# Kernel optimization log

Hardware: AMD Instinct MI355X
Metric: run time of the kernel (lower is better)

The kernel has to match this reference:

```python
import jax, jax.numpy as jnp
import numpy as np

K_HOPS = 3  # spektral TAGConv default
BN_EPS = 1e-3  # keras BatchNormalization default epsilon


def _propagate(x, edge_src, edge_dst, edge_weight, n_nodes):
    # y[dst] += w * x[src]  (sparse adjacency @ x)
    msg = x[edge_src] * edge_weight[:, None]
    return jax.ops.segment_sum(msg, edge_dst, num_segments=n_nodes)


def _tag_conv(x, edge_src, edge_dst, edge_weight, W, b):
    n = x.shape[0]
    hops = [x]
    h = x
    for _ in range(K_HOPS):
        h = _propagate(h, edge_src, edge_dst, edge_weight, n)
        hops.append(h)
    # concat hops along features then dense combine: [N, F*(K+1)] @ [F*(K+1), C]
    return jnp.concatenate(hops, axis=-1) @ W + b


def setup_inputs() -> dict:
    key = jax.random.key(0)
    ks = jax.random.split(key, 6)
    N, F, E, H, L = 20000, 2000, 640000, 128, 15
    x = jax.random.normal(ks[0], (N, F), dtype=jnp.float32)
    edge_src = jax.random.randint(ks[1], (E,), 0, N, dtype=jnp.int32)
    edge_dst = jax.random.randint(ks[2], (E,), 0, N, dtype=jnp.int32)
    # normalized adjacency weights, roughly 1/avg_degree scale
    edge_weight = jax.random.uniform(ks[3], (E,), dtype=jnp.float32) / 32.0
    W1 = jax.random.normal(ks[4], (F * (K_HOPS + 1), H), dtype=jnp.float32) * (1.0 / np.sqrt(F * (K_HOPS + 1)))
    b1 = jnp.zeros((H,), dtype=jnp.float32)
    gamma = jnp.ones((H,), dtype=jnp.float32)
    beta = jnp.zeros((H,), dtype=jnp.float32)
    moving_mean = jnp.zeros((H,), dtype=jnp.float32)
    moving_var = jnp.ones((H,), dtype=jnp.float32)
    W2 = jax.random.normal(ks[5], (H * (K_HOPS + 1), L), dtype=jnp.float32) * (1.0 / np.sqrt(H * (K_HOPS + 1)))
    b2 = jnp.zeros((L,), dtype=jnp.float32)
    return {"x": x, "edge_src": edge_src, "edge_dst": edge_dst, "edge_weight": edge_weight,
            "W1": W1, "b1": b1, "gamma": gamma, "beta": beta,
            "moving_mean": moving_mean, "moving_var": moving_var, "W2": W2, "b2": b2}


def reference(x, edge_src, edge_dst, edge_weight, W1, b1, gamma, beta,
              moving_mean, moving_var, W2, b2):
    # training=False: Dropout is identity, BN uses moving statistics
    h = _tag_conv(x, edge_src, edge_dst, edge_weight, W1, b1)
    h = (h - moving_mean) * jax.lax.rsqrt(moving_var + BN_EPS) * gamma + beta
    h = jax.nn.relu(h)
    z = _tag_conv(h, edge_src, edge_dst, edge_weight, W2, b2)
    return z
```

## Files before the change

kernel.cpp:

```cpp
#include <hip/hip_runtime.h>
#include <hip/hip_bf16.h>
#include <cstdint>
#include <cstddef>

#define N_NODES 20000
#define F_IN    2000
#define H_DIM   128
#define L_DIM   15
#define K_PAD   2048
#define YS      384
#define BM      128
#define BN      64
#define BK      32
#define I_TILES 157

typedef __attribute__((ext_vector_type(4))) float f32x4;
typedef __attribute__((ext_vector_type(8))) short s16x8;
typedef __attribute__((ext_vector_type(8))) unsigned short u16x8;

__device__ __forceinline__ unsigned short f2bf(float f) {
  unsigned int u = __float_as_uint(f);
  u += 0x7fff + ((u >> 16) & 1);
  return (unsigned short)(u >> 16);
}

__device__ __forceinline__ unsigned int pkbf(float a, float b) {
  union { __hip_bfloat162 h; unsigned int u; } cv;
  cv.h = __float22bfloat162_rn(make_float2(a, b));
  return cv.u;
}

__device__ __forceinline__ float2 bf2f(unsigned int u) {
  float2 r;
  r.x = __uint_as_float(u << 16);
  r.y = __uint_as_float(u & 0xffff0000u);
  return r;
}

__global__ __launch_bounds__(256) void k_cvt_x(const float* __restrict__ x,
                                               unsigned short* __restrict__ xb) {
  unsigned int t = blockIdx.x * 256u + threadIdx.x;
  unsigned int row = t >> 8;
  unsigned int colB = (t & 255u) * 8u;
  u16x8 o = {0, 0, 0, 0, 0, 0, 0, 0};
  if (colB < F_IN) {
    const float4 a = *(const float4*)(x + (size_t)row * F_IN + colB);
    const float4 b = *(const float4*)(x + (size_t)row * F_IN + colB + 4);
    o[0] = f2bf(a.x); o[1] = f2bf(a.y); o[2] = f2bf(a.z); o[3] = f2bf(a.w);
    o[4] = f2bf(b.x); o[5] = f2bf(b.y); o[6] = f2bf(b.z); o[7] = f2bf(b.w);
  }
  *(u16x8*)(xb + (size_t)t * 8) = o;
}

__global__ __launch_bounds__(256) void k_cvt_w1(const float* __restrict__ W1,
                                                unsigned short* __restrict__ bt) {
  __shared__ unsigned short tile[128 * 67];
  const int hop = blockIdx.x >> 5;
  const int k0  = (blockIdx.x & 31) * 64;
  const int t = threadIdx.x;
#pragma unroll
  for (int it = 0; it < 8; ++it) {
    int f4 = it * 256 + t;
    int r  = f4 >> 5;
    int c4 = f4 & 31;
    int k = k0 + r;
    float4 v = make_float4(0.f, 0.f, 0.f, 0.f);
    if (k < F_IN) v = *(const float4*)(W1 + (size_t)(hop * F_IN + k) * H_DIM + c4 * 4);
    tile[(c4 * 4 + 0) * 67 + r] = f2bf(v.x);
    tile[(c4 * 4 + 1) * 67 + r] = f2bf(v.y);
    tile[(c4 * 4 + 2) * 67 + r] = f2bf(v.z);
    tile[(c4 * 4 + 3) * 67 + r] = f2bf(v.w);
  }
  __syncthreads();
  const int c = t >> 1, kh = (t & 1) * 32;
  unsigned short* dst = bt + (size_t)(hop * 128 + c) * K_PAD + k0 + kh;
  const unsigned short* srcp = tile + c * 67 + kh;
#pragma unroll
  for (int q = 0; q < 4; ++q) {
    u16x8 o;
#pragma unroll
    for (int e = 0; e < 8; ++e) o[e] = srcp[q * 8 + e];
    *(u16x8*)(dst + q * 8) = o;
  }
}

__global__ __launch_bounds__(256) void k_gemm1(const unsigned short* __restrict__ A,
                                               const unsigned short* __restrict__ B,
                                               float* __restrict__ Y,
                                               unsigned short* __restrict__ Yb3) {
  __shared__ unsigned short As[BM * BK];
  __shared__ unsigned short Bs[BN * BK];
  const int b = blockIdx.x;
  const int i_tile = (b & 7) + 8 * (b >> 6);
  const int j_tile = (b >> 3) & 7;
  if (i_tile >= I_TILES) return;
  const int rowA0 = i_tile * BM;
  const int colB0 = j_tile * BN;
  const int tid  = threadIdx.x;
  const int lane = tid & 63;
  const int wave = tid >> 6;
  const int wm = (wave >> 1) * 64;
  const int wn = (wave & 1) * 32;
  const int quad = lane >> 4;
  const int l15  = lane & 15;
  f32x4 acc[4][2] = {};

  for (int kt = 0; kt < K_PAD; kt += BK) {
#pragma unroll
    for (int r = 0; r < 2; ++r) {
      int c = r * 256 + tid;
      int row = c >> 2;
      int kc = (c & 3) * 8;
      const unsigned short* ga = A + (size_t)(rowA0 + row) * K_PAD + kt + kc;
      __builtin_amdgcn_global_load_lds((const __attribute__((address_space(1))) void*)ga,
                                       (__attribute__((address_space(3))) void*)(As + c * 8),
                                       16, 0, 0);
    }
    {
      int c = tid;
      int row = c >> 2;
      int kc = (c & 3) * 8;
      const unsigned short* gb = B + (size_t)(colB0 + row) * K_PAD + kt + kc;
      __builtin_amdgcn_global_load_lds((const __attribute__((address_space(1))) void*)gb,
                                       (__attribute__((address_space(3))) void*)(Bs + c * 8),
                                       16, 0, 0);
    }
    __syncthreads();
    s16x8 af[4], bfr[2];
#pragma unroll
    for (int i = 0; i < 4; ++i)
      af[i] = *(const s16x8*)(As + (wm + i * 16 + l15) * BK + quad * 8);
#pragma unroll
    for (int j = 0; j < 2; ++j)
      bfr[j] = *(const s16x8*)(Bs + (wn + j * 16 + l15) * BK + quad * 8);
#pragma unroll
    for (int i = 0; i < 4; ++i)
#pragma unroll
      for (int j = 0; j < 2; ++j)
        acc[i][j] = __builtin_amdgcn_mfma_f32_16x16x32_bf16(af[i], bfr[j], acc[i][j], 0, 0, 0);
    __syncthreads();
  }

#pragma unroll
  for (int i = 0; i < 4; ++i) {
    int row0 = rowA0 + wm + i * 16 + quad * 4;
#pragma unroll
    for (int j = 0; j < 2; ++j) {
      int gcol = colB0 + wn + j * 16 + l15;
#pragma unroll
      for (int r = 0; r < 4; ++r) {
        int row = row0 + r;
        if (row < N_NODES) {
          if (j_tile < 6)
            Y[(size_t)row * YS + gcol] = acc[i][j][r];
          else
            Yb3[(size_t)row * H_DIM + (gcol - 384)] = f2bf(acc[i][j][r]);
        }
      }
    }
  }
}

__global__ __launch_bounds__(256) void k_hist(const int* __restrict__ dst,
                                              int* __restrict__ deg, int E) {
  int i = blockIdx.x * 256 + threadIdx.x;
  int e = i * 4;
  if (e + 4 <= E) {
    int4 d4 = *(const int4*)(dst + e);
    atomicAdd(&deg[d4.x], 1); atomicAdd(&deg[d4.y], 1);
    atomicAdd(&deg[d4.z], 1); atomicAdd(&deg[d4.w], 1);
  } else {
    for (; e < E; ++e) atomicAdd(&deg[dst[e]], 1);
  }
}

__global__ __launch_bounds__(1024) void k_scan(const int* __restrict__ deg,
                                               int* __restrict__ rowStart,
                                               int* __restrict__ cursor) {
  __shared__ int sums[1024];
  const int t = threadIdx.x;
  const int chunk = (N_NODES + 1023) / 1024;
  int lo = t * chunk;
  int hi = lo + chunk; if (hi > N_NODES) hi = N_NODES;
  int s = 0;
  for (int i = lo; i < hi; ++i) s += deg[i];
  sums[t] = s;
  __syncthreads();
  for (int off = 1; off < 1024; off <<= 1) {
    int v = sums[t];
    int u = (t >= off) ? sums[t - off] : 0;
    __syncthreads();
    sums[t] = v + u;
    __syncthreads();
  }
  int run = sums[t] - s;
  for (int i = lo; i < hi; ++i) {
    rowStart[i] = run; cursor[i] = run; run += deg[i];
  }
  if (t == 1023) rowStart[N_NODES] = run;
}

__global__ __launch_bounds__(256) void k_scatter(const int* __restrict__ src,
                                                 const int* __restrict__ dst,
                                                 const float* __restrict__ w,
                                                 int* cursor,
                                                 int2* __restrict__ eSW, int E) {
  int e = blockIdx.x * 256 + threadIdx.x;
  if (e >= E) return;
  int p = atomicAdd(&cursor[dst[e]], 1);
  eSW[p] = make_int2(src[e], __float_as_int(w[e]));
}

__global__ __launch_bounds__(256) void k_prop128e(const int* __restrict__ rowStart,
    const int2* __restrict__ eSW,
    const unsigned short* __restrict__ gsrc,
    const float* __restrict__ addv, int addStride, int addOff,
    unsigned short* __restrict__ outb, float* __restrict__ outf,
    const float* __restrict__ b1, const float* __restrict__ gamma,
    const float* __restrict__ beta, const float* __restrict__ mean,
    const float* __restrict__ var, int doBN) {
  const int lane = threadIdx.x & 63;
  const int wave = threadIdx.x >> 6;
  const int h   = lane >> 5;
  const int sub = lane & 31;
  const int d = blockIdx.x * 4 + wave;
  const int s0 = rowStart[d], s1 = rowStart[d + 1];
  f32x4 acc = {0.f, 0.f, 0.f, 0.f};

  const int nc = (s1 - s0) >> 4;
  int j = s0;
  int2 ed[8];
  if (nc > 0) {
#pragma unroll
    for (int i = 0; i < 8; ++i) ed[i] = eSW[j + 2 * i + h];
  }
  for (int c = 0; c < nc; ++c) {
    uint2 g[8];
#pragma unroll
    for (int i = 0; i < 8; ++i)
      g[i] = *(const uint2*)(gsrc + (size_t)ed[i].x * H_DIM + sub * 4);
    int2 edn[8];
    if (c + 1 < nc) {
#pragma unroll
      for (int i = 0; i < 8; ++i) edn[i] = eSW[j + 16 + 2 * i + h];
    }
#pragma unroll
    for (int i = 0; i < 8; ++i) {
      float w = __int_as_float(ed[i].y);
      float2 lo = bf2f(g[i].x), hi = bf2f(g[i].y);
      acc.x = fmaf(w, lo.x, acc.x); acc.y = fmaf(w, lo.y, acc.y);
      acc.z = fmaf(w, hi.x, acc.z); acc.w = fmaf(w, hi.y, acc.w);
    }
    if (c + 1 < nc) {
#pragma unroll
      for (int i = 0; i < 8; ++i) ed[i] = edn[i];
    }
    j += 16;
  }
  for (int t = s0 + nc * 16 + h; t < s1; t += 2) {
    int2 e = eSW[t];
    uint2 g = *(const uint2*)(gsrc + (size_t)e.x * H_DIM + sub * 4);
    float w = __int_as_float(e.y);
    float2 lo = bf2f(g.x), hi = bf2f(g.y);
    acc.x = fmaf(w, lo.x, acc.x); acc.y = fmaf(w, lo.y, acc.y);
    acc.z = fmaf(w, hi.x, acc.z); acc.w = fmaf(w, hi.y, acc.w);
  }
  acc.x += __shfl_xor(acc.x, 32);
  acc.y += __shfl_xor(acc.y, 32);
  acc.z += __shfl_xor(acc.z, 32);
  acc.w += __shfl_xor(acc.w, 32);
  if (h) return;
  const int c4 = sub * 4;
  float4 av = *(const float4*)(addv + (size_t)d * addStride + addOff + c4);
  float r0 = av.x + acc.x, r1 = av.y + acc.y;
  float r2 = av.z + acc.z, r3 = av.w + acc.w;
  if (doBN) {
    float4 bb = *(const float4*)(b1 + c4);
    float4 gg = *(const float4*)(gamma + c4);
    float4 be = *(const float4*)(beta + c4);
    float4 mm = *(const float4*)(mean + c4);
    float4 vv = *(const float4*)(var + c4);
    r0 = (r0 + bb.x - mm.x) * rsqrtf(vv.x + 1e-3f) * gg.x + be.x;
    r1 = (r1 + bb.y - mm.y) * rsqrtf(vv.y + 1e-3f) * gg.y + be.y;
    r2 = (r2 + bb.z - mm.z) * rsqrtf(vv.z + 1e-3f) * gg.z + be.z;
    r3 = (r3 + bb.w - mm.w) * rsqrtf(vv.w + 1e-3f) * gg.w + be.w;
    r0 = r0 > 0.f ? r0 : 0.f; r1 = r1 > 0.f ? r1 : 0.f;
    r2 = r2 > 0.f ? r2 : 0.f; r3 = r3 > 0.f ? r3 : 0.f;
    *(float4*)(outf + (size_t)d * H_DIM + c4) = make_float4(r0, r1, r2, r3);
  } else {
    *(uint2*)(outb + (size_t)d * H_DIM + c4) = make_uint2(pkbf(r0, r1), pkbf(r2, r3));
  }
}

__global__ __launch_bounds__(256) void k_gemm2(const float* __restrict__ Hh,
                                               const float* __restrict__ W2,
                                               float* __restrict__ Y2) {
  __shared__ float w2s[512 * 15];
  for (int i = threadIdx.x; i < 512 * 15; i += 256) w2s[i] = W2[i];
  __syncthreads();
  const int c = threadIdx.x & 63;
  const int d = blockIdx.x * 4 + (threadIdx.x >> 6);
  if (c >= 60 || d >= N_NODES) return;
  const int hop = c / 15, j = c % 15;
  const float4* hr4 = (const float4*)(Hh + (size_t)d * H_DIM);
  float acc = 0.f;
#pragma unroll 8
  for (int k4 = 0; k4 < 32; ++k4) {
    float4 h = hr4[k4];
    const float* wp = w2s + ((hop << 7) + k4 * 4) * 15 + j;
    acc = fmaf(h.x, wp[0],  acc);
    acc = fmaf(h.y, wp[15], acc);
    acc = fmaf(h.z, wp[30], acc);
    acc = fmaf(h.w, wp[45], acc);
  }
  Y2[(size_t)d * 60 + c] = acc;
}

__global__ __launch_bounds__(256) void k_prop15(const int* __restrict__ rowStart,
    const int2* __restrict__ eSW,
    const float* __restrict__ in, int inStride, int inOff,
    const float* __restrict__ addv, int addStride, int addOff,
    const float* __restrict__ bias, float* __restrict__ out) {
  const int f = threadIdx.x & 15;
  const int d = blockIdx.x * 16 + (threadIdx.x >> 4);
  if (f >= 15) return;
  const int s0 = rowStart[d], s1 = rowStart[d + 1];
  float acc = 0.f;
  int j = s0;
  for (; j + 4 <= s1; j += 4) {
    int2 e0 = eSW[j], e1 = eSW[j + 1], e2 = eSW[j + 2], e3 = eSW[j + 3];
    float v0 = in[(size_t)e0.x * inStride + inOff + f];
    float v1 = in[(size_t)e1.x * inStride + inOff + f];
    float v2 = in[(size_t)e2.x * inStride + inOff + f];
    float v3 = in[(size_t)e3.x * inStride + inOff + f];
    acc = fmaf(__int_as_float(e0.y), v0, acc);
    acc = fmaf(__int_as_float(e1.y), v1, acc);
    acc = fmaf(__int_as_float(e2.y), v2, acc);
    acc = fmaf(__int_as_float(e3.y), v3, acc);
  }
  for (; j < s1; ++j) {
    int2 e = eSW[j];
    acc = fmaf(__int_as_float(e.y), in[(size_t)e.x * inStride + inOff + f], acc);
  }
  float b = bias ? bias[f] : 0.f;
  out[(size_t)d * 15 + f] = addv[(size_t)d * addStride + addOff + f] + acc + b;
}

extern "C" void kernel_launch(void* const* d_in, const int* in_sizes, int n_in,
                              void* d_out, int out_size, void* d_ws, size_t ws_size,
                              hipStream_t stream) {
  const float* x     = (const float*)d_in[0];
  const int*   esrc  = (const int*)d_in[1];
  const int*   edst  = (const int*)d_in[2];
  const float* ew    = (const float*)d_in[3];
  const float* W1    = (const float*)d_in[4];
  const float* b1    = (const float*)d_in[5];
  const float* gamma = (const float*)d_in[6];
  const float* beta  = (const float*)d_in[7];
  const float* mmean = (const float*)d_in[8];
  const float* mvar  = (const float*)d_in[9];
  const float* W2    = (const float*)d_in[10];
  const float* b2    = (const float*)d_in[11];
  const int E = in_sizes[1];
  char* ws = (char*)d_ws;

  unsigned short* xb  = (unsigned short*)(ws);
  float*          Y   = (float*)(ws + 81920000);
  unsigned short* Yb3 = (unsigned short*)(ws + 112640000);
  unsigned short* w1r = (unsigned short*)(ws + 117760000);
  int2*           eSW = (int2*)(ws + 119857152);
  int*       deg      = (int*)(ws + 124977152);
  int*       rowStart = (int*)(ws + 125057280);
  int*       cursor   = (int*)(ws + 125137408);
  unsigned short* P   = (unsigned short*)(ws);
  unsigned short* Q   = (unsigned short*)(ws + 5120000);
  float*          Hb  = (float*)(ws + 10240000);
  float*          Y2  = (float*)(ws + 20480000);
  float*          zP  = (float*)(ws + 25280000);
  float*          zQ  = (float*)(ws + 26480000);
  float*          zout = (float*)d_out;

  hipMemsetAsync(deg, 0, N_NODES * sizeof(int), stream);

  k_hist<<<(E / 4 + 255) / 256 + 1, 256, 0, stream>>>(edst, deg, E);
  k_scan<<<1, 1024, 0, stream>>>(deg, rowStart, cursor);
  k_scatter<<<(E + 255) / 256, 256, 0, stream>>>(esrc, edst, ew, cursor, eSW, E);

  k_cvt_x<<<(N_NODES * K_PAD / 8) / 256, 256, 0, stream>>>(x, xb);
  k_cvt_w1<<<128, 256, 0, stream>>>(W1, w1r);
  k_gemm1<<<1280, 256, 0, stream>>>(xb, w1r, Y, Yb3);

  k_prop128e<<<N_NODES / 4, 256, 0, stream>>>(rowStart, eSW, Yb3, Y, YS, 256,
                                              P, nullptr, b1, gamma, beta, mmean, mvar, 0);
  k_prop128e<<<N_NODES / 4, 256, 0, stream>>>(rowStart, eSW, P, Y, YS, 128,
                                              Q, nullptr, b1, gamma, beta, mmean, mvar, 0);
  k_prop128e<<<N_NODES / 4, 256, 0, stream>>>(rowStart, eSW, Q, Y, YS, 0,
                                              nullptr, Hb, b1, gamma, beta, mmean, mvar, 1);

  k_gemm2<<<N_NODES / 4, 256, 0, stream>>>(Hb, W2, Y2);
  k_prop15<<<N_NODES / 16, 256, 0, stream>>>(rowStart, eSW, Y2, 60, 45, Y2, 60, 30, nullptr, zP);
  k_prop15<<<N_NODES / 16, 256, 0, stream>>>(rowStart, eSW, zP, 15, 0, Y2, 60, 15, nullptr, zQ);
  k_prop15<<<N_NODES / 16, 256, 0, stream>>>(rowStart, eSW, zQ, 15, 0, Y2, 60, 0, b2, zout);
}
```

Baseline: 604.6 us.

## Pad CSR rows to multiples of 16 and widen per-lane gathers to 16 bytes

The CSR build now rounds each node's edge segment up to a multiple of 16. A new kernel fills the padding slots with zero-weight dummy edges pointing at node 0, so the 128-wide propagation kernel no longer needs a scalar tail loop. The propagation kernel is also reorganised so that 16 lanes cover a row with 16-byte bf16 loads and 4 edges are handled per wave step, followed by a two-stage shuffle reduction. This removes the divergent tail and halves the number of gather instructions, at the cost of extra padded edge traffic, one more small kernel, and a larger edge buffer.

```diff
diff --git a/kernel.cpp b/kernel.cpp
--- a/kernel.cpp
+++ b/kernel.cpp
@@ -176,14 +176,15 @@
 
 __global__ __launch_bounds__(1024) void k_scan(const int* __restrict__ deg,
                                                int* __restrict__ rowStart,
-                                               int* __restrict__ cursor) {
+                                               int* __restrict__ cursor,
+                                               int* __restrict__ realEnd) {
   __shared__ int sums[1024];
   const int t = threadIdx.x;
   const int chunk = (N_NODES + 1023) / 1024;
   int lo = t * chunk;
   int hi = lo + chunk; if (hi > N_NODES) hi = N_NODES;
   int s = 0;
-  for (int i = lo; i < hi; ++i) s += deg[i];
+  for (int i = lo; i < hi; ++i) s += (deg[i] + 15) & ~15;
   sums[t] = s;
   __syncthreads();
   for (int off = 1; off < 1024; off <<= 1) {
@@ -195,7 +196,8 @@
   }
   int run = sums[t] - s;
   for (int i = lo; i < hi; ++i) {
-    rowStart[i] = run; cursor[i] = run; run += deg[i];
+    rowStart[i] = run; cursor[i] = run; realEnd[i] = run + deg[i];
+    run += (deg[i] + 15) & ~15;
   }
   if (t == 1023) rowStart[N_NODES] = run;
 }
@@ -211,7 +213,17 @@
   eSW[p] = make_int2(src[e], __float_as_int(w[e]));
 }
 
-__global__ __launch_bounds__(256) void k_prop128e(const int* __restrict__ rowStart,
+__global__ __launch_bounds__(256) void k_pad(const int* __restrict__ rowStart,
+                                             const int* __restrict__ realEnd,
+                                             int2* __restrict__ eSW) {
+  int t = blockIdx.x * 256 + threadIdx.x;
+  int d = t >> 4, i = t & 15;
+  if (d >= N_NODES) return;
+  int s = realEnd[d] + i;
+  if (s < rowStart[d + 1]) eSW[s] = make_int2(0, 0);
+}
+
+__global__ __launch_bounds__(256) void k_prop128f(const int* __restrict__ rowStart,
     const int2* __restrict__ eSW,
     const unsigned short* __restrict__ gsrc,
     const float* __restrict__ addv, int addStride, int addOff,
@@ -221,74 +233,82 @@
     const float* __restrict__ var, int doBN) {
   const int lane = threadIdx.x & 63;
   const int wave = threadIdx.x >> 6;
-  const int h   = lane >> 5;
-  const int sub = lane & 31;
+  const int eidx = lane >> 4;
+  const int s16  = lane & 15;
   const int d = blockIdx.x * 4 + wave;
   const int s0 = rowStart[d], s1 = rowStart[d + 1];
-  f32x4 acc = {0.f, 0.f, 0.f, 0.f};
+  f32x4 a0 = {0.f, 0.f, 0.f, 0.f};
+  f32x4 a1 = {0.f, 0.f, 0.f, 0.f};
 
   const int nc = (s1 - s0) >> 4;
   int j = s0;
-  int2 ed[8];
+  int2 ed0[4], ed1[4];
   if (nc > 0) {
 #pragma unroll
-    for (int i = 0; i < 8; ++i) ed[i] = eSW[j + 2 * i + h];
+    for (int i = 0; i < 4; ++i) ed0[i] = eSW[j + 4 * i + eidx];
   }
   for (int c = 0; c < nc; ++c) {
-    uint2 g[8];
-#pragma unroll
-    for (int i = 0; i < 8; ++i)
-      g[i] = *(const uint2*)(gsrc + (size_t)ed[i].x * H_DIM + sub * 4);
-    int2 edn[8];
+    uint4 g[4];
+#pragma unroll
+    for (int i = 0; i < 4; ++i)
+      g[i] = *(const uint4*)(gsrc + (size_t)ed0[i].x * H_DIM + s16 * 8);
     if (c + 1 < nc) {
 #pragma unroll
-      for (int i = 0; i < 8; ++i) edn[i] = eSW[j + 16 + 2 * i + h];
+      for (int i = 0; i < 4; ++i) ed1[i] = eSW[j + 16 + 4 * i + eidx];
     }
 #pragma unroll
-    for (int i = 0; i < 8; ++i) {
-      float w = __int_as_float(ed[i].y);
-      float2 lo = bf2f(g[i].x), hi = bf2f(g[i].y);
-      acc.x = fmaf(w, lo.x, acc.x); acc.y = fmaf(w, lo.y, acc.y);
-      acc.z = fmaf(w, hi.x, acc.z); acc.w = fmaf(w, hi.y, acc.w);
+    for (int i = 0; i < 4; ++i) {
+      float w = __int_as_float(ed0[i].y);
+      float2 p0 = bf2f(g[i].x), p1 = bf2f(g[i].y);
+      float2 p2 = bf2f(g[i].z), p3 = bf2f(g[i].w);
+      a0.x = fmaf(w, p0.x, a0.x); a0.y = fmaf(w, p0.y, a0.y);
+      a0.z = fmaf(w, p1.x, a0.z); a0.w = fmaf(w, p1.y, a0.w);
+      a1.x = fmaf(w, p2.x, a1.x); a1.y = fmaf(w, p2.y, a1.y);
+      a1.z = fmaf(w, p3.x, a1.z); a1.w = fmaf(w, p3.y, a1.w);
     }
-    if (c + 1 < nc) {
-#pragma unroll
-      for (int i = 0; i < 8; ++i) ed[i] = edn[i];
-    }
+#pragma unroll
+    for (int i = 0; i < 4; ++i) ed0[i] = ed1[i];
     j += 16;
   }
-  for (int t = s0 + nc * 16 + h; t < s1; t += 2) {
-    int2 e = eSW[t];
-    uint2 g = *(const uint2*)(gsrc + (size_t)e.x * H_DIM + sub * 4);
-    float w = __int_as_float(e.y);
-    float2 lo = bf2f(g.x), hi = bf2f(g.y);
-    acc.x = fmaf(w, lo.x, acc.x); acc.y = fmaf(w, lo.y, acc.y);
-    acc.z = fmaf(w, hi.x, acc.z); acc.w = fmaf(w, hi.y, acc.w);
-  }
-  acc.x += __shfl_xor(acc.x, 32);
-  acc.y += __shfl_xor(acc.y, 32);
-  acc.z += __shfl_xor(acc.z, 32);
-  acc.w += __shfl_xor(acc.w, 32);
-  if (h) return;
-  const int c4 = sub * 4;
-  float4 av = *(const float4*)(addv + (size_t)d * addStride + addOff + c4);
-  float r0 = av.x + acc.x, r1 = av.y + acc.y;
-  float r2 = av.z + acc.z, r3 = av.w + acc.w;
+  a0.x += __shfl_xor(a0.x, 16); a0.y += __shfl_xor(a0.y, 16);
+  a0.z += __shfl_xor(a0.z, 16); a0.w += __shfl_xor(a0.w, 16);
+  a1.x += __shfl_xor(a1.x, 16); a1.y += __shfl_xor(a1.y, 16);
+  a1.z += __shfl_xor(a1.z, 16); a1.w += __shfl_xor(a1.w, 16);
+  a0.x += __shfl_xor(a0.x, 32); a0.y += __shfl_xor(a0.y, 32);
+  a0.z += __shfl_xor(a0.z, 32); a0.w += __shfl_xor(a0.w, 32);
+  a1.x += __shfl_xor(a1.x, 32); a1.y += __shfl_xor(a1.y, 32);
+  a1.z += __shfl_xor(a1.z, 32); a1.w += __shfl_xor(a1.w, 32);
+  if (lane >= 16) return;
+  const int c8 = s16 * 8;
+  const float* ap = addv + (size_t)d * addStride + addOff + c8;
+  float4 av0 = *(const float4*)ap;
+  float4 av1 = *(const float4*)(ap + 4);
+  float r0 = av0.x + a0.x, r1 = av0.y + a0.y, r2 = av0.z + a0.z, r3 = av0.w + a0.w;
+  float r4 = av1.x + a1.x, r5 = av1.y + a1.y, r6 = av1.z + a1.z, r7 = av1.w + a1.w;
   if (doBN) {
-    float4 bb = *(const float4*)(b1 + c4);
-    float4 gg = *(const float4*)(gamma + c4);
-    float4 be = *(const float4*)(beta + c4);
-    float4 mm = *(const float4*)(mean + c4);
-    float4 vv = *(const float4*)(var + c4);
-    r0 = (r0 + bb.x - mm.x) * rsqrtf(vv.x + 1e-3f) * gg.x + be.x;
-    r1 = (r1 + bb.y - mm.y) * rsqrtf(vv.y + 1e-3f) * gg.y + be.y;
-    r2 = (r2 + bb.z - mm.z) * rsqrtf(vv.z + 1e-3f) * gg.z + be.z;
-    r3 = (r3 + bb.w - mm.w) * rsqrtf(vv.w + 1e-3f) * gg.w + be.w;
+    float4 bb0 = *(const float4*)(b1 + c8),    bb1 = *(const float4*)(b1 + c8 + 4);
+    float4 gg0 = *(const float4*)(gamma + c8), gg1 = *(const float4*)(gamma + c8 + 4);
+    float4 be0 = *(const float4*)(beta + c8),  be1 = *(const float4*)(beta + c8 + 4);
+    float4 mm0 = *(const float4*)(mean + c8),  mm1 = *(const float4*)(mean + c8 + 4);
+    float4 vv0 = *(const float4*)(var + c8),   vv1 = *(const float4*)(var + c8 + 4);
+    r0 = (r0 + bb0.x - mm0.x) * rsqrtf(vv0.x + 1e-3f) * gg0.x + be0.x;
+    r1 = (r1 + bb0.y - mm0.y) * rsqrtf(vv0.y + 1e-3f) * gg0.y + be0.y;
+    r2 = (r2 + bb0.z - mm0.z) * rsqrtf(vv0.z + 1e-3f) * gg0.z + be0.z;
+    r3 = (r3 + bb0.w - mm0.w) * rsqrtf(vv0.w + 1e-3f) * gg0.w + be0.w;
+    r4 = (r4 + bb1.x - mm1.x) * rsqrtf(vv1.x + 1e-3f) * gg1.x + be1.x;
+    r5 = (r5 + bb1.y - mm1.y) * rsqrtf(vv1.y + 1e-3f) * gg1.y + be1.y;
+    r6 = (r6 + bb1.z - mm1.z) * rsqrtf(vv1.z + 1e-3f) * gg1.z + be1.z;
+    r7 = (r7 + bb1.w - mm1.w) * rsqrtf(vv1.w + 1e-3f) * gg1.w + be1.w;
     r0 = r0 > 0.f ? r0 : 0.f; r1 = r1 > 0.f ? r1 : 0.f;
     r2 = r2 > 0.f ? r2 : 0.f; r3 = r3 > 0.f ? r3 : 0.f;
-    *(float4*)(outf + (size_t)d * H_DIM + c4) = make_float4(r0, r1, r2, r3);
+    r4 = r4 > 0.f ? r4 : 0.f; r5 = r5 > 0.f ? r5 : 0.f;
+    r6 = r6 > 0.f ? r6 : 0.f; r7 = r7 > 0.f ? r7 : 0.f;
+    float* op = outf + (size_t)d * H_DIM + c8;
+    *(float4*)op = make_float4(r0, r1, r2, r3);
+    *(float4*)(op + 4) = make_float4(r4, r5, r6, r7);
   } else {
-    *(uint2*)(outb + (size_t)d * H_DIM + c4) = make_uint2(pkbf(r0, r1), pkbf(r2, r3));
+    *(uint4*)(outb + (size_t)d * H_DIM + c8) =
+        make_uint4(pkbf(r0, r1), pkbf(r2, r3), pkbf(r4, r5), pkbf(r6, r7));
   }
 }
 
@@ -369,9 +389,10 @@
   unsigned short* Yb3 = (unsigned short*)(ws + 112640000);
   unsigned short* w1r = (unsigned short*)(ws + 117760000);
   int2*           eSW = (int2*)(ws + 119857152);
-  int*       deg      = (int*)(ws + 124977152);
-  int*       rowStart = (int*)(ws + 125057280);
-  int*       cursor   = (int*)(ws + 125137408);
+  int*       deg      = (int*)(ws + 127537152);
+  int*       rowStart = (int*)(ws + 127617280);
+  int*       cursor   = (int*)(ws + 127697408);
+  int*       realEnd  = (int*)(ws + 127777536);
   unsigned short* P   = (unsigned short*)(ws);
   unsigned short* Q   = (unsigned short*)(ws + 5120000);
   float*          Hb  = (float*)(ws + 10240000);
@@ -383,18 +404,19 @@
   hipMemsetAsync(deg, 0, N_NODES * sizeof(int), stream);
 
   k_hist<<<(E / 4 + 255) / 256 + 1, 256, 0, stream>>>(edst, deg, E);
-  k_scan<<<1, 1024, 0, stream>>>(deg, rowStart, cursor);
+  k_scan<<<1, 1024, 0, stream>>>(deg, rowStart, cursor, realEnd);
   k_scatter<<<(E + 255) / 256, 256, 0, stream>>>(esrc, edst, ew, cursor, eSW, E);
+  k_pad<<<(N_NODES * 16) / 256, 256, 0, stream>>>(rowStart, realEnd, eSW);
 
   k_cvt_x<<<(N_NODES * K_PAD / 8) / 256, 256, 0, stream>>>(x, xb);
   k_cvt_w1<<<128, 256, 0, stream>>>(W1, w1r);
   k_gemm1<<<1280, 256, 0, stream>>>(xb, w1r, Y, Yb3);
 
-  k_prop128e<<<N_NODES / 4, 256, 0, stream>>>(rowStart, eSW, Yb3, Y, YS, 256,
+  k_prop128f<<<N_NODES / 4, 256, 0, stream>>>(rowStart, eSW, Yb3, Y, YS, 256,
                                               P, nullptr, b1, gamma, beta, mmean, mvar, 0);
-  k_prop128e<<<N_NODES / 4, 256, 0, stream>>>(rowStart, eSW, P, Y, YS, 128,
+  k_prop128f<<<N_NODES / 4, 256, 0, stream>>>(rowStart, eSW, P, Y, YS, 128,
                                               Q, nullptr, b1, gamma, beta, mmean, mvar, 0);
-  k_prop128e<<<N_NODES / 4, 256, 0, stream>>>(rowStart, eSW, Q, Y, YS, 0,
+  k_prop128f<<<N_NODES / 4, 256, 0, stream>>>(rowStart, eSW, Q, Y, YS, 0,
                                               nullptr, Hb, b1, gamma, beta, mmean, mvar, 1);
 
   k_gemm2<<<N_NODES / 4, 256, 0, stream>>>(Hb, W2, Y2);
```

Measured after the change: 582.6 us. -3.6%, faster.
